# Kernel tuning notes

Measured on AMD Instinct MI355X. Metric: run time of the kernel, lower is better.

Reference implementation:

```python
import jax, jax.numpy as jnp
import numpy as np

B, L, D = 4, 4096, 256


def setup_inputs() -> dict:
    key = jax.random.key(0)
    kx, kq, kk, kv, ko = jax.random.split(key, 5)
    std = 0.02
    return {
        "x": jax.random.normal(kx, (B, L, D), dtype=jnp.float32),
        "Wq": std * jax.random.normal(kq, (D, D), dtype=jnp.float32),
        "Wk": std * jax.random.normal(kk, (D, D), dtype=jnp.float32),
        "Wv": std * jax.random.normal(kv, (D, D), dtype=jnp.float32),
        "Wo": std * jax.random.normal(ko, (D, D), dtype=jnp.float32),
    }


def reference(x, Wq, Wk, Wv, Wo):
    # nn.Linear(d,d,bias=False): y = x @ W.T
    q = x @ Wq.T  # [B,L,D]
    k = x @ Wk.T
    v = x @ Wv.T
    logits = jnp.einsum("bld,bmd->blm", q, k)  # [B,L,L], no 1/sqrt(d) scaling
    Lq = x.shape[1]
    causal_mask = jnp.triu(jnp.ones((Lq, Lq), dtype=bool), k=1)  # True above diag
    # ReLU attention: mask future to 0, relu, divide row i by max(i, 1)
    logits = jnp.where(causal_mask[None], jnp.asarray(0.0, logits.dtype), logits)
    attn = jax.nn.relu(logits)
    row_counts = jnp.maximum(jnp.arange(Lq, dtype=attn.dtype), 1.0)  # clamp_min(1)
    attn = attn / row_counts[None, :, None]
    ctx = jnp.einsum("blm,bmd->bld", attn, v)
    return ctx @ Wo.T
```

## Files before the change

### kernel.cpp

```cpp
#include <hip/hip_runtime.h>

#define BB 4
#define LL 4096
#define DD 256
#define MAXOFF 80

typedef short bf16x8 __attribute__((ext_vector_type(8)));
typedef short bf16x4 __attribute__((ext_vector_type(4)));
typedef float f32x4 __attribute__((ext_vector_type(4)));
typedef unsigned u32x4 __attribute__((ext_vector_type(4)));
typedef unsigned short u16;

__device__ inline u16 f2b(float f) {
    union { float f; unsigned u; } v; v.f = f;
    unsigned r = (v.u + 0x7fffu + ((v.u >> 16) & 1u)) >> 16;
    return (u16)r;
}
__device__ inline float b2f(short s) {
    union { unsigned u; float f; } v; v.u = ((unsigned)(unsigned short)s) << 16;
    return v.f;
}
__device__ inline unsigned pk2(float lo, float hi) {
    union { float f; unsigned u; } a, b; a.f = lo; b.f = hi;
    return __builtin_amdgcn_perm(b.u, a.u, 0x07060302u);
}

__device__ inline f32x4 mfma32(bf16x8 a, bf16x8 b, f32x4 c) {
    return __builtin_amdgcn_mfma_f32_16x16x32_bf16(a, b, c, 0, 0, 0);
}
__device__ inline f32x4 mfma16(bf16x4 a, bf16x4 b, f32x4 c) {
    return __builtin_amdgcn_mfma_f32_16x16x16bf16_1k(a, b, c, 0, 0, 0);
}

__device__ inline void gl_lds(const u16* g, u16* l) {
    __builtin_amdgcn_global_load_lds(
        (const __attribute__((address_space(1))) void*)g,
        (__attribute__((address_space(3))) void*)l, 16, 0, 0);
}


__global__ __launch_bounds__(256) void wconv_kernel(
    const float* __restrict__ Wq, const float* __restrict__ Wk,
    const float* __restrict__ Wv, const float* __restrict__ Wo,
    u16* __restrict__ wf, u16* __restrict__ wo16)
{
    const int w = threadIdx.x >> 6, lane = threadIdx.x & 63;
    const int q4 = lane >> 4, ln = lane & 15;
    const int id = blockIdx.x * 4 + w;
    const int mat = id >> 7, rem = id & 127, ct = rem >> 3, ks = rem & 7;
    if (mat < 3) {
        const float* W = (mat == 0) ? Wq : (mat == 1) ? Wk : Wv;
        const float* src = W + (size_t)(ct * 16 + ln) * DD + ks * 32 + q4 * 8;
        float4 f0 = ((const float4*)src)[0], f1 = ((const float4*)src)[1];
        bf16x8 t;
        t[0] = (short)f2b(f0.x); t[1] = (short)f2b(f0.y);
        t[2] = (short)f2b(f0.z); t[3] = (short)f2b(f0.w);
        t[4] = (short)f2b(f1.x); t[5] = (short)f2b(f1.y);
        t[6] = (short)f2b(f1.z); t[7] = (short)f2b(f1.w);
        *(bf16x8*)(wf + (size_t)mat * 65536 + (ct * 8 + ks) * 512 + lane * 8) = t;
    } else {
        const float* src = Wo + (size_t)(ct * 16 + ln) * DD + ks * 32 + q4 * 4;
        float4 f0 = *(const float4*)src;
        float4 f1 = *(const float4*)(src + 16);
        bf16x4 t0, t1;
        t0[0] = (short)f2b(f0.x); t0[1] = (short)f2b(f0.y);
        t0[2] = (short)f2b(f0.z); t0[3] = (short)f2b(f0.w);
        t1[0] = (short)f2b(f1.x); t1[1] = (short)f2b(f1.y);
        t1[2] = (short)f2b(f1.z); t1[3] = (short)f2b(f1.w);
        *(bf16x4*)(wo16 + (size_t)(ct * 16 + 2 * ks) * 256 + lane * 4) = t0;
        *(bf16x4*)(wo16 + (size_t)(ct * 16 + 2 * ks + 1) * 256 + lane * 4) = t1;
    }
}

__global__ __launch_bounds__(256, 4) void qkv_kernel(
    const float* __restrict__ x, const u16* __restrict__ wf,
    u16* __restrict__ qf, u16* __restrict__ kf_, u16* __restrict__ vf_)
{
    __shared__ u16 lt_q[32 * 136];
    __shared__ u16 lt_k[32 * 136];
    __shared__ u16 lt_v[128 * 40];

    const int w = threadIdx.x >> 6, lane = threadIdx.x & 63;
    const int q4 = lane >> 4, ln = lane & 15;
    const int tg = blockIdx.x >> 1, half = blockIdx.x & 1;
    const int tl = w & 1, dq = w >> 1;

    bf16x8 a[8];
    {
        const float* xrow = x + (size_t)(tg * 32 + tl * 16 + ln) * DD;
        #pragma unroll
        for (int ks = 0; ks < 8; ++ks) {
            const float4* p = (const float4*)(xrow + ks * 32 + q4 * 8);
            float4 f0 = p[0], f1 = p[1];
            bf16x8 t;
            t[0] = (short)f2b(f0.x); t[1] = (short)f2b(f0.y);
            t[2] = (short)f2b(f0.z); t[3] = (short)f2b(f0.w);
            t[4] = (short)f2b(f1.x); t[5] = (short)f2b(f1.y);
            t[6] = (short)f2b(f1.z); t[7] = (short)f2b(f1.w);
            a[ks] = t;
        }
    }

    f32x4 acc0[4], acc1[4], acc2[4];
    #pragma unroll
    for (int cl = 0; cl < 4; ++cl) {
        acc0[cl] = f32x4{0.f, 0.f, 0.f, 0.f};
        acc1[cl] = f32x4{0.f, 0.f, 0.f, 0.f};
        acc2[cl] = f32x4{0.f, 0.f, 0.f, 0.f};
    }

    #pragma unroll
    for (int ks = 0; ks < 8; ++ks) {
        #pragma unroll
        for (int cl = 0; cl < 4; ++cl) {
            const int ct = half * 8 + dq * 4 + cl;
            const size_t off = ((size_t)ct * 8 + ks) * 512 + lane * 8;
            bf16x8 b0 = *(const bf16x8*)(wf + off);
            bf16x8 b1 = *(const bf16x8*)(wf + 65536 + off);
            bf16x8 b2 = *(const bf16x8*)(wf + 131072 + off);
            acc0[cl] = mfma32(a[ks], b0, acc0[cl]);
            acc1[cl] = mfma32(a[ks], b1, acc1[cl]);
            acc2[cl] = mfma32(a[ks], b2, acc2[cl]);
        }
    }

    #pragma unroll
    for (int cl = 0; cl < 4; ++cl) {
        const int coll = (dq * 4 + cl) * 16 + ln;
        #pragma unroll
        for (int r = 0; r < 4; ++r) {
            const int tok = tl * 16 + q4 * 4 + r;
            lt_q[tok * 136 + coll] = f2b(acc0[cl][r]);
            lt_k[tok * 136 + coll] = f2b(acc1[cl][r]);
            lt_v[coll * 40 + tok] = f2b(acc2[cl][r]);
        }
    }
    __syncthreads();

    {
        const int h = w & 1;
        #pragma unroll
        for (int e = 0; e < 2; ++e) {
            const int ksl = 2 * dq + e;
            const int ks = half * 4 + ksl;
            bf16x8 aq = *(const bf16x8*)&lt_q[(h * 16 + ln) * 136 + ksl * 32 + q4 * 8];
            bf16x8 ak = *(const bf16x8*)&lt_k[(h * 16 + ln) * 136 + ksl * 32 + q4 * 8];
            const size_t dst = (size_t)((tg * 2 + h) * 8 + ks) * 512 + lane * 8;
            *(bf16x8*)(qf + dst) = aq;
            *(bf16x8*)(kf_ + dst) = ak;
        }
    }
    #pragma unroll
    for (int e = 0; e < 2; ++e) {
        const int dt_l = 2 * w + e;
        bf16x4 lo = *(const bf16x4*)&lt_v[(dt_l * 16 + ln) * 40 + q4 * 4];
        bf16x4 hi = *(const bf16x4*)&lt_v[(dt_l * 16 + ln) * 40 + 16 + q4 * 4];
        bf16x8 t;
        t[0] = lo[0]; t[1] = lo[1]; t[2] = lo[2]; t[3] = lo[3];
        t[4] = hi[0]; t[5] = hi[1]; t[6] = hi[2]; t[7] = hi[3];
        *(bf16x8*)(vf_ + (size_t)(tg * 16 + half * 8 + dt_l) * 512 + lane * 8) = t;
    }
}

__global__ __launch_bounds__(512, 2) void attn_kernel(
    const u16* __restrict__ qf, const u16* __restrict__ kfr,
    const u16* __restrict__ vfr, u16* __restrict__ part)
{
    __shared__ u16 buf[2][32][512];

    const int id = blockIdx.x;
    const int xcd = id & 7;
    const int b = xcd >> 1;
    const int j = ((xcd & 1) << 5) | (id >> 3);

    const int w = threadIdx.x >> 6, lane = threadIdx.x & 63;
    const int q4 = lane >> 4, ln = lane & 15;

    const int u0 = 17 * j;
    const int u1 = u0 + 17;

    int g = (int)((sqrtf((float)u0 + 1.0f) - 1.0f) * 0.5f);
    while (4 * (g + 1) * (g + 2) <= u0) ++g;
    while (4 * g * (g + 1) > u0) --g;
    int kt = u0 - 4 * g * (g + 1);
    int u = u0;

    int off = 0;
    for (int g2 = 0; g2 < g; ++g2) {
        const int j0 = (4 * g2 * (g2 + 1)) / 17;
        const int jl = (4 * (g2 + 1) * (g2 + 2) - 1) / 17;
        off += jl - j0 + 1;
    }

    {
        const size_t cb = (size_t)((b * 128 + kt) * 16) * 512;
        #pragma unroll
        for (int c4 = 0; c4 < 4; ++c4) {
            const int c = w * 4 + c4;
            const u16* gsrc = ((c < 16) ? (kfr + cb + c * 512)
                                        : (vfr + cb + (c - 16) * 512)) + lane * 8;
            gl_lds(gsrc, &buf[u0 & 1][c][0]);
        }
    }

    while (u < u1) {
        const int ktend = 8 * g + 8;
        const int rem = u1 - u;
        const int kt_stop = (ktend < kt + rem) ? ktend : (kt + rem);
        const int t0 = g * 16 + 2 * w;
        const int qg0 = t0 * 16 + ln;
        const float inv0 = 1.0f / (float)(qg0 > 1 ? qg0 : 1);
        const float inv1 = 1.0f / (float)(qg0 + 16);

        bf16x8 qB0[8], qB1[8];
        {
            const u16* qb0 = qf + (size_t)(t0 * 8) * 512 + (size_t)b * (128 * 16 * 512) + lane * 8;
            #pragma unroll
            for (int ks = 0; ks < 8; ++ks) {
                qB0[ks] = *(const bf16x8*)(qb0 + ks * 512);
                qB1[ks] = *(const bf16x8*)(qb0 + (8 + ks) * 512);
            }
        }

        f32x4 oacc0[16], oacc1[16];
        #pragma unroll
        for (int dt = 0; dt < 16; ++dt) {
            oacc0[dt] = f32x4{0.f, 0.f, 0.f, 0.f};
            oacc1[dt] = f32x4{0.f, 0.f, 0.f, 0.f};
        }

        #pragma unroll 1
        for (; kt < kt_stop; ++kt, ++u) {
            const int cur = u & 1;
            __syncthreads();

            if (u + 1 < u1) {
                const int ktn = (kt + 1 < ktend) ? (kt + 1) : 0;
                const size_t cb = (size_t)((b * 128 + ktn) * 16) * 512;
                #pragma unroll
                for (int c4 = 0; c4 < 4; ++c4) {
                    const int c = w * 4 + c4;
                    const u16* gsrc = ((c < 16) ? (kfr + cb + c * 512)
                                                : (vfr + cb + (c - 16) * 512)) + lane * 8;
                    gl_lds(gsrc, &buf[cur ^ 1][c][0]);
                }
            }

            f32x4 s00 = f32x4{0.f, 0.f, 0.f, 0.f};
            f32x4 s10 = f32x4{0.f, 0.f, 0.f, 0.f};
            f32x4 s01 = f32x4{0.f, 0.f, 0.f, 0.f};
            f32x4 s11 = f32x4{0.f, 0.f, 0.f, 0.f};
            #pragma unroll
            for (int ks = 0; ks < 8; ++ks) {
                bf16x8 kf0 = *(const bf16x8*)&buf[cur][ks][lane * 8];
                bf16x8 kf1 = *(const bf16x8*)&buf[cur][8 + ks][lane * 8];
                s00 = mfma32(kf0, qB0[ks], s00);
                s10 = mfma32(kf1, qB0[ks], s10);
                s01 = mfma32(kf0, qB1[ks], s01);
                s11 = mfma32(kf1, qB1[ks], s11);
            }

            const int d0 = kt * 32 + q4 * 4 - qg0;
            float v00[4], v10[4], v01[4], v11[4];
            #pragma unroll
            for (int rr = 0; rr < 4; ++rr) {
                v00[rr] = (d0 + rr > 0)      ? 0.f : fmaxf(s00[rr], 0.f) * inv0;
                v10[rr] = (d0 + 16 + rr > 0) ? 0.f : fmaxf(s10[rr], 0.f) * inv0;
                v01[rr] = (d0 - 16 + rr > 0) ? 0.f : fmaxf(s01[rr], 0.f) * inv1;
                v11[rr] = (d0 + rr > 0)      ? 0.f : fmaxf(s11[rr], 0.f) * inv1;
            }
            union { u32x4 u; bf16x8 h; } c0, c1;
            c0.u[0] = pk2(v00[0], v00[1]); c0.u[1] = pk2(v00[2], v00[3]);
            c0.u[2] = pk2(v10[0], v10[1]); c0.u[3] = pk2(v10[2], v10[3]);
            c1.u[0] = pk2(v01[0], v01[1]); c1.u[1] = pk2(v01[2], v01[3]);
            c1.u[2] = pk2(v11[0], v11[1]); c1.u[3] = pk2(v11[2], v11[3]);

            #pragma unroll
            for (int dt = 0; dt < 16; ++dt) {
                bf16x8 vv = *(const bf16x8*)&buf[cur][16 + dt][lane * 8];
                oacc0[dt] = mfma32(vv, c0.h, oacc0[dt]);
                oacc1[dt] = mfma32(vv, c1.h, oacc1[dt]);
            }
        }

        {
            const int j0g = (4 * g * (g + 1)) / 17;
            const int gslot = off + (j - j0g);
            u16* pb0 = part + ((((size_t)b * MAXOFF + gslot) * 16 + 2 * w) * 16) * 256 + lane * 4;
            u16* pb1 = pb0 + 16 * 256;
            #pragma unroll
            for (int dt = 0; dt < 16; ++dt) {
                bf16x4 t0v, t1v;
                t0v[0] = (short)f2b(oacc0[dt][0]); t0v[1] = (short)f2b(oacc0[dt][1]);
                t0v[2] = (short)f2b(oacc0[dt][2]); t0v[3] = (short)f2b(oacc0[dt][3]);
                t1v[0] = (short)f2b(oacc1[dt][0]); t1v[1] = (short)f2b(oacc1[dt][1]);
                t1v[2] = (short)f2b(oacc1[dt][2]); t1v[3] = (short)f2b(oacc1[dt][3]);
                *(bf16x4*)(pb0 + dt * 256) = t0v;
                *(bf16x4*)(pb1 + dt * 256) = t1v;
            }
            off += ((4 * (g + 1) * (g + 2) - 1) / 17) - j0g + 1;
        }
        ++g;
        kt = 0;
    }
}

__global__ __launch_bounds__(256, 4) void oproj_kernel(
    const u16* __restrict__ part, const u16* __restrict__ wo16,
    float* __restrict__ out)
{
    __shared__ u16 cb[16 * 256];

    const int w = threadIdx.x >> 6, lane = threadIdx.x & 63;
    const int q4 = lane >> 4, ln = lane & 15;
    const int g16 = blockIdx.x;
    const int b = g16 >> 8, gb = g16 & 255;
    const int g = gb >> 4;
    const int tloc = gb & 15;

    int off = 0;
    for (int g2 = 0; g2 < g; ++g2) {
        const int j0 = (4 * g2 * (g2 + 1)) / 17;
        const int jl = (4 * (g2 + 1) * (g2 + 2) - 1) / 17;
        off += jl - j0 + 1;
    }
    const int j0g = (4 * g * (g + 1)) / 17;
    const int jlg = (4 * (g + 1) * (g + 2) - 1) / 17;
    const int nsl = jlg - j0g + 1;

    #pragma unroll
    for (int c4 = 0; c4 < 4; ++c4) {
        const int dt = w * 4 + c4;
        f32x4 s = f32x4{0.f, 0.f, 0.f, 0.f};
        for (int sl = 0; sl < nsl; ++sl) {
            const u16* p = part + ((((size_t)b * MAXOFF + off + sl) * 16 + tloc) * 16 + dt) * 256 + lane * 4;
            bf16x4 pv = *(const bf16x4*)p;
            s[0] += b2f(pv[0]); s[1] += b2f(pv[1]);
            s[2] += b2f(pv[2]); s[3] += b2f(pv[3]);
        }
        bf16x4 t;
        t[0] = (short)f2b(s[0]); t[1] = (short)f2b(s[1]);
        t[2] = (short)f2b(s[2]); t[3] = (short)f2b(s[3]);
        *(bf16x4*)&cb[dt * 256 + lane * 4] = t;
    }
    __syncthreads();

    #pragma unroll
    for (int c4 = 0; c4 < 4; ++c4) {
        const int ct = w * 4 + c4;
        f32x4 acc = f32x4{0.f, 0.f, 0.f, 0.f};
        #pragma unroll
        for (int dt = 0; dt < 16; ++dt) {
            bf16x4 A = *(const bf16x4*)(wo16 + (size_t)(ct * 16 + dt) * 256 + lane * 4);
            bf16x4 B = *(const bf16x4*)&cb[dt * 256 + lane * 4];
            acc = mfma16(A, B, acc);
        }
        float* o = out + (size_t)(g16 * 16 + ln) * DD + ct * 16 + q4 * 4;
        *(f32x4*)o = acc;
    }
}

extern "C" void kernel_launch(void* const* d_in, const int* in_sizes, int n_in,
                              void* d_out, int out_size, void* d_ws, size_t ws_size,
                              hipStream_t stream)
{
    const float* x  = (const float*)d_in[0];
    const float* Wq = (const float*)d_in[1];
    const float* Wk = (const float*)d_in[2];
    const float* Wv = (const float*)d_in[3];
    const float* Wo = (const float*)d_in[4];
    float* out = (float*)d_out;

    const size_t nW = (size_t)DD * DD;
    const size_t nX = (size_t)BB * LL * DD;

    u16* wf   = (u16*)d_ws;
    u16* wo16 = wf + 3 * nW;
    u16* qfr  = wf + 4 * nW;
    u16* kfr  = qfr + nX;
    u16* vfr  = kfr + nX;
    u16* part = vfr + nX;

    wconv_kernel<<<dim3(128), dim3(256), 0, stream>>>(Wq, Wk, Wv, Wo, wf, wo16);
    qkv_kernel<<<dim3(1024), dim3(256), 0, stream>>>(x, wf, qfr, kfr, vfr);
    attn_kernel<<<dim3(256), dim3(512), 0, stream>>>(qfr, kfr, vfr, part);
    oproj_kernel<<<dim3(1024), dim3(256), 0, stream>>>(part, wo16, out);
}
```

Baseline: 153.9 us.

## Give each attention wave four query tiles, halving the block to four waves

The attention kernel now runs 256 threads (4 waves) per block instead of 512, and each wave handles four 16-row query tiles instead of two. Each K/V fragment read from LDS now feeds twice as many MFMAs, which cuts LDS read traffic per FLOP. Each wave also issues twice as many global-to-LDS copies. The cost is roughly double the accumulator and Q register footprint (64 f32x4 accumulators plus 32 Q fragments per lane) and fewer waves per CU for hiding latency, so register spilling or lower occupancy is a risk.

New measurement: 168.3 us. 9.3% more time.

```diff
diff --git a/kernel.cpp b/kernel.cpp
--- a/kernel.cpp
+++ b/kernel.cpp
@@ -162,7 +162,7 @@
     }
 }
 
-__global__ __launch_bounds__(512, 2) void attn_kernel(
+__global__ __launch_bounds__(256, 1) void attn_kernel(
     const u16* __restrict__ qf, const u16* __restrict__ kfr,
     const u16* __restrict__ vfr, u16* __restrict__ part)
 {
@@ -195,8 +195,8 @@
     {
         const size_t cb = (size_t)((b * 128 + kt) * 16) * 512;
         #pragma unroll
-        for (int c4 = 0; c4 < 4; ++c4) {
-            const int c = w * 4 + c4;
+        for (int c8 = 0; c8 < 8; ++c8) {
+            const int c = w * 8 + c8;
             const u16* gsrc = ((c < 16) ? (kfr + cb + c * 512)
                                         : (vfr + cb + (c - 16) * 512)) + lane * 8;
             gl_lds(gsrc, &buf[u0 & 1][c][0]);
@@ -207,27 +207,31 @@
         const int ktend = 8 * g + 8;
         const int rem = u1 - u;
         const int kt_stop = (ktend < kt + rem) ? ktend : (kt + rem);
-        const int t0 = g * 16 + 2 * w;
+        const int t0 = g * 16 + 4 * w;
         const int qg0 = t0 * 16 + ln;
-        const float inv0 = 1.0f / (float)(qg0 > 1 ? qg0 : 1);
-        const float inv1 = 1.0f / (float)(qg0 + 16);
-
-        bf16x8 qB0[8], qB1[8];
+        float inv[4];
+        inv[0] = 1.0f / (float)(qg0 > 1 ? qg0 : 1);
+        inv[1] = 1.0f / (float)(qg0 + 16);
+        inv[2] = 1.0f / (float)(qg0 + 32);
+        inv[3] = 1.0f / (float)(qg0 + 48);
+
+        bf16x8 qB[4][8];
         {
             const u16* qb0 = qf + (size_t)(t0 * 8) * 512 + (size_t)b * (128 * 16 * 512) + lane * 8;
             #pragma unroll
-            for (int ks = 0; ks < 8; ++ks) {
-                qB0[ks] = *(const bf16x8*)(qb0 + ks * 512);
-                qB1[ks] = *(const bf16x8*)(qb0 + (8 + ks) * 512);
-            }
-        }
-
-        f32x4 oacc0[16], oacc1[16];
-        #pragma unroll
-        for (int dt = 0; dt < 16; ++dt) {
-            oacc0[dt] = f32x4{0.f, 0.f, 0.f, 0.f};
-            oacc1[dt] = f32x4{0.f, 0.f, 0.f, 0.f};
-        }
+            for (int qfg = 0; qfg < 4; ++qfg) {
+                #pragma unroll
+                for (int ks = 0; ks < 8; ++ks)
+                    qB[qfg][ks] = *(const bf16x8*)(qb0 + (qfg * 8 + ks) * 512);
+            }
+        }
+
+        f32x4 oacc[4][16];
+        #pragma unroll
+        for (int qfg = 0; qfg < 4; ++qfg)
+            #pragma unroll
+            for (int dt = 0; dt < 16; ++dt)
+                oacc[qfg][dt] = f32x4{0.f, 0.f, 0.f, 0.f};
 
         #pragma unroll 1
         for (; kt < kt_stop; ++kt, ++u) {
@@ -238,65 +242,69 @@
                 const int ktn = (kt + 1 < ktend) ? (kt + 1) : 0;
                 const size_t cb = (size_t)((b * 128 + ktn) * 16) * 512;
                 #pragma unroll
-                for (int c4 = 0; c4 < 4; ++c4) {
-                    const int c = w * 4 + c4;
+                for (int c8 = 0; c8 < 8; ++c8) {
+                    const int c = w * 8 + c8;
                     const u16* gsrc = ((c < 16) ? (kfr + cb + c * 512)
                                                 : (vfr + cb + (c - 16) * 512)) + lane * 8;
                     gl_lds(gsrc, &buf[cur ^ 1][c][0]);
                 }
             }
 
-            f32x4 s00 = f32x4{0.f, 0.f, 0.f, 0.f};
-            f32x4 s10 = f32x4{0.f, 0.f, 0.f, 0.f};
-            f32x4 s01 = f32x4{0.f, 0.f, 0.f, 0.f};
-            f32x4 s11 = f32x4{0.f, 0.f, 0.f, 0.f};
+            f32x4 s0[4], s1[4];
+            #pragma unroll
+            for (int qfg = 0; qfg < 4; ++qfg) {
+                s0[qfg] = f32x4{0.f, 0.f, 0.f, 0.f};
+                s1[qfg] = f32x4{0.f, 0.f, 0.f, 0.f};
+            }
             #pragma unroll
             for (int ks = 0; ks < 8; ++ks) {
                 bf16x8 kf0 = *(const bf16x8*)&buf[cur][ks][lane * 8];
                 bf16x8 kf1 = *(const bf16x8*)&buf[cur][8 + ks][lane * 8];
-                s00 = mfma32(kf0, qB0[ks], s00);
-                s10 = mfma32(kf1, qB0[ks], s10);
-                s01 = mfma32(kf0, qB1[ks], s01);
-                s11 = mfma32(kf1, qB1[ks], s11);
+                #pragma unroll
+                for (int qfg = 0; qfg < 4; ++qfg) {
+                    s0[qfg] = mfma32(kf0, qB[qfg][ks], s0[qfg]);
+                    s1[qfg] = mfma32(kf1, qB[qfg][ks], s1[qfg]);
+                }
             }
 
             const int d0 = kt * 32 + q4 * 4 - qg0;
-            float v00[4], v10[4], v01[4], v11[4];
-            #pragma unroll
-            for (int rr = 0; rr < 4; ++rr) {
-                v00[rr] = (d0 + rr > 0)      ? 0.f : fmaxf(s00[rr], 0.f) * inv0;
-                v10[rr] = (d0 + 16 + rr > 0) ? 0.f : fmaxf(s10[rr], 0.f) * inv0;
-                v01[rr] = (d0 - 16 + rr > 0) ? 0.f : fmaxf(s01[rr], 0.f) * inv1;
-                v11[rr] = (d0 + rr > 0)      ? 0.f : fmaxf(s11[rr], 0.f) * inv1;
-            }
-            union { u32x4 u; bf16x8 h; } c0, c1;
-            c0.u[0] = pk2(v00[0], v00[1]); c0.u[1] = pk2(v00[2], v00[3]);
-            c0.u[2] = pk2(v10[0], v10[1]); c0.u[3] = pk2(v10[2], v10[3]);
-            c1.u[0] = pk2(v01[0], v01[1]); c1.u[1] = pk2(v01[2], v01[3]);
-            c1.u[2] = pk2(v11[0], v11[1]); c1.u[3] = pk2(v11[2], v11[3]);
+            union { u32x4 u; bf16x8 h; } c[4];
+            #pragma unroll
+            for (int qfg = 0; qfg < 4; ++qfg) {
+                float v0[4], v1[4];
+                #pragma unroll
+                for (int rr = 0; rr < 4; ++rr) {
+                    v0[rr] = (d0 - 16 * qfg + rr > 0)      ? 0.f : fmaxf(s0[qfg][rr], 0.f) * inv[qfg];
+                    v1[rr] = (d0 + 16 - 16 * qfg + rr > 0) ? 0.f : fmaxf(s1[qfg][rr], 0.f) * inv[qfg];
+                }
+                c[qfg].u[0] = pk2(v0[0], v0[1]); c[qfg].u[1] = pk2(v0[2], v0[3]);
+                c[qfg].u[2] = pk2(v1[0], v1[1]); c[qfg].u[3] = pk2(v1[2], v1[3]);
+            }
 
             #pragma unroll
             for (int dt = 0; dt < 16; ++dt) {
                 bf16x8 vv = *(const bf16x8*)&buf[cur][16 + dt][lane * 8];
-                oacc0[dt] = mfma32(vv, c0.h, oacc0[dt]);
-                oacc1[dt] = mfma32(vv, c1.h, oacc1[dt]);
+                #pragma unroll
+                for (int qfg = 0; qfg < 4; ++qfg)
+                    oacc[qfg][dt] = mfma32(vv, c[qfg].h, oacc[qfg][dt]);
             }
         }
 
         {
             const int j0g = (4 * g * (g + 1)) / 17;
             const int gslot = off + (j - j0g);
-            u16* pb0 = part + ((((size_t)b * MAXOFF + gslot) * 16 + 2 * w) * 16) * 256 + lane * 4;
-            u16* pb1 = pb0 + 16 * 256;
-            #pragma unroll
-            for (int dt = 0; dt < 16; ++dt) {
-                bf16x4 t0v, t1v;
-                t0v[0] = (short)f2b(oacc0[dt][0]); t0v[1] = (short)f2b(oacc0[dt][1]);
-                t0v[2] = (short)f2b(oacc0[dt][2]); t0v[3] = (short)f2b(oacc0[dt][3]);
-                t1v[0] = (short)f2b(oacc1[dt][0]); t1v[1] = (short)f2b(oacc1[dt][1]);
-                t1v[2] = (short)f2b(oacc1[dt][2]); t1v[3] = (short)f2b(oacc1[dt][3]);
-                *(bf16x4*)(pb0 + dt * 256) = t0v;
-                *(bf16x4*)(pb1 + dt * 256) = t1v;
+            #pragma unroll
+            for (int qfg = 0; qfg < 4; ++qfg) {
+                u16* pb = part + ((((size_t)b * MAXOFF + gslot) * 16 + (4 * w + qfg)) * 16) * 256 + lane * 4;
+                #pragma unroll
+                for (int dt = 0; dt < 16; ++dt) {
+                    bf16x4 t;
+                    t[0] = (short)f2b(oacc[qfg][dt][0]);
+                    t[1] = (short)f2b(oacc[qfg][dt][1]);
+                    t[2] = (short)f2b(oacc[qfg][dt][2]);
+                    t[3] = (short)f2b(oacc[qfg][dt][3]);
+                    *(bf16x4*)(pb + dt * 256) = t;
+                }
             }
             off += ((4 * (g + 1) * (g + 2) - 1) / 17) - j0g + 1;
         }
@@ -383,6 +391,6 @@
 
     wconv_kernel<<<dim3(128), dim3(256), 0, stream>>>(Wq, Wk, Wv, Wo, wf, wo16);
     qkv_kernel<<<dim3(1024), dim3(256), 0, stream>>>(x, wf, qfr, kfr, vfr);
-    attn_kernel<<<dim3(256), dim3(512), 0, stream>>>(qfr, kfr, vfr, part);
+    attn_kernel<<<dim3(256), dim3(256), 0, stream>>>(qfr, kfr, vfr, part);
     oproj_kernel<<<dim3(1024), dim3(256), 0, stream>>>(part, wo16, out);
 }
```

## Triple-buffer K/V tiles in attention and widen QKV blocks to full width

Applied to the files above, without the earlier changes.

The attention kernel moves from double to triple buffering of K/V tiles. It prefetches two tiles ahead and replaces the per-iteration __syncthreads with an explicit vmcnt wait plus s_barrier, so global loads overlap more with MFMA work. The QKV projection kernel now uses 512-thread blocks that each compute all 256 output columns, so each x row is loaded and converted to bf16 once instead of twice. The trade-off is that the attention kernel now needs 96KB of LDS per block, which may cut blocks per CU. The hand-tuned vmcnt count also depends on how many loads are still in flight.

Measured after the change: 165.1 us. 1.07x slower.

```diff
diff --git a/kernel.cpp b/kernel.cpp
--- a/kernel.cpp
+++ b/kernel.cpp
@@ -72,17 +72,17 @@
     }
 }
 
-__global__ __launch_bounds__(256, 4) void qkv_kernel(
+__global__ __launch_bounds__(512, 2) void qkv_kernel(
     const float* __restrict__ x, const u16* __restrict__ wf,
     u16* __restrict__ qf, u16* __restrict__ kf_, u16* __restrict__ vf_)
 {
-    __shared__ u16 lt_q[32 * 136];
-    __shared__ u16 lt_k[32 * 136];
-    __shared__ u16 lt_v[128 * 40];
+    __shared__ u16 lt_q[32 * 264];
+    __shared__ u16 lt_k[32 * 264];
+    __shared__ u16 lt_v[256 * 40];
 
     const int w = threadIdx.x >> 6, lane = threadIdx.x & 63;
     const int q4 = lane >> 4, ln = lane & 15;
-    const int tg = blockIdx.x >> 1, half = blockIdx.x & 1;
+    const int tg = blockIdx.x;
     const int tl = w & 1, dq = w >> 1;
 
     bf16x8 a[8];
@@ -113,7 +113,7 @@
     for (int ks = 0; ks < 8; ++ks) {
         #pragma unroll
         for (int cl = 0; cl < 4; ++cl) {
-            const int ct = half * 8 + dq * 4 + cl;
+            const int ct = dq * 4 + cl;
             const size_t off = ((size_t)ct * 8 + ks) * 512 + lane * 8;
             bf16x8 b0 = *(const bf16x8*)(wf + off);
             bf16x8 b1 = *(const bf16x8*)(wf + 65536 + off);
@@ -130,21 +130,20 @@
         #pragma unroll
         for (int r = 0; r < 4; ++r) {
             const int tok = tl * 16 + q4 * 4 + r;
-            lt_q[tok * 136 + coll] = f2b(acc0[cl][r]);
-            lt_k[tok * 136 + coll] = f2b(acc1[cl][r]);
+            lt_q[tok * 264 + coll] = f2b(acc0[cl][r]);
+            lt_k[tok * 264 + coll] = f2b(acc1[cl][r]);
             lt_v[coll * 40 + tok] = f2b(acc2[cl][r]);
         }
     }
     __syncthreads();
 
     {
-        const int h = w & 1;
+        const int h = tl;
         #pragma unroll
         for (int e = 0; e < 2; ++e) {
-            const int ksl = 2 * dq + e;
-            const int ks = half * 4 + ksl;
-            bf16x8 aq = *(const bf16x8*)&lt_q[(h * 16 + ln) * 136 + ksl * 32 + q4 * 8];
-            bf16x8 ak = *(const bf16x8*)&lt_k[(h * 16 + ln) * 136 + ksl * 32 + q4 * 8];
+            const int ks = 2 * dq + e;
+            bf16x8 aq = *(const bf16x8*)&lt_q[(h * 16 + ln) * 264 + ks * 32 + q4 * 8];
+            bf16x8 ak = *(const bf16x8*)&lt_k[(h * 16 + ln) * 264 + ks * 32 + q4 * 8];
             const size_t dst = (size_t)((tg * 2 + h) * 8 + ks) * 512 + lane * 8;
             *(bf16x8*)(qf + dst) = aq;
             *(bf16x8*)(kf_ + dst) = ak;
@@ -152,13 +151,13 @@
     }
     #pragma unroll
     for (int e = 0; e < 2; ++e) {
-        const int dt_l = 2 * w + e;
-        bf16x4 lo = *(const bf16x4*)&lt_v[(dt_l * 16 + ln) * 40 + q4 * 4];
-        bf16x4 hi = *(const bf16x4*)&lt_v[(dt_l * 16 + ln) * 40 + 16 + q4 * 4];
+        const int dt = 2 * w + e;
+        bf16x4 lo = *(const bf16x4*)&lt_v[(dt * 16 + ln) * 40 + q4 * 4];
+        bf16x4 hi = *(const bf16x4*)&lt_v[(dt * 16 + ln) * 40 + 16 + q4 * 4];
         bf16x8 t;
         t[0] = lo[0]; t[1] = lo[1]; t[2] = lo[2]; t[3] = lo[3];
         t[4] = hi[0]; t[5] = hi[1]; t[6] = hi[2]; t[7] = hi[3];
-        *(bf16x8*)(vf_ + (size_t)(tg * 16 + half * 8 + dt_l) * 512 + lane * 8) = t;
+        *(bf16x8*)(vf_ + (size_t)(tg * 16 + dt) * 512 + lane * 8) = t;
     }
 }
 
@@ -166,7 +165,7 @@
     const u16* __restrict__ qf, const u16* __restrict__ kfr,
     const u16* __restrict__ vfr, u16* __restrict__ part)
 {
-    __shared__ u16 buf[2][32][512];
+    __shared__ u16 buf[3][32][512];
 
     const int id = blockIdx.x;
     const int xcd = id & 7;
@@ -192,16 +191,23 @@
         off += jl - j0 + 1;
     }
 
-    {
-        const size_t cb = (size_t)((b * 128 + kt) * 16) * 512;
+    int lg = g, lkt = kt;
+    int cur = 0;
+
+    auto issue = [&](int bi) {
+        const size_t cb = (size_t)((b * 128 + lkt) * 16) * 512;
         #pragma unroll
         for (int c4 = 0; c4 < 4; ++c4) {
             const int c = w * 4 + c4;
             const u16* gsrc = ((c < 16) ? (kfr + cb + c * 512)
                                         : (vfr + cb + (c - 16) * 512)) + lane * 8;
-            gl_lds(gsrc, &buf[u0 & 1][c][0]);
-        }
-    }
+            gl_lds(gsrc, &buf[bi][c][0]);
+        }
+        ++lkt; if (lkt == 8 * lg + 8) { lkt = 0; ++lg; }
+    };
+
+    issue(0);
+    if (u0 + 1 < u1) issue(1);
 
     while (u < u1) {
         const int ktend = 8 * g + 8;
@@ -231,19 +237,13 @@
 
         #pragma unroll 1
         for (; kt < kt_stop; ++kt, ++u) {
-            const int cur = u & 1;
-            __syncthreads();
-
-            if (u + 1 < u1) {
-                const int ktn = (kt + 1 < ktend) ? (kt + 1) : 0;
-                const size_t cb = (size_t)((b * 128 + ktn) * 16) * 512;
-                #pragma unroll
-                for (int c4 = 0; c4 < 4; ++c4) {
-                    const int c = w * 4 + c4;
-                    const u16* gsrc = ((c < 16) ? (kfr + cb + c * 512)
-                                                : (vfr + cb + (c - 16) * 512)) + lane * 8;
-                    gl_lds(gsrc, &buf[cur ^ 1][c][0]);
-                }
+            asm volatile("s_waitcnt vmcnt(4)" ::: "memory");
+            __builtin_amdgcn_s_barrier();
+            asm volatile("" ::: "memory");
+
+            if (u + 2 < u1) {
+                const int nb = (cur + 2 >= 3) ? (cur - 1) : (cur + 2);
+                issue(nb);
             }
 
             f32x4 s00 = f32x4{0.f, 0.f, 0.f, 0.f};
@@ -281,6 +281,8 @@
                 oacc0[dt] = mfma32(vv, c0.h, oacc0[dt]);
                 oacc1[dt] = mfma32(vv, c1.h, oacc1[dt]);
             }
+
+            cur = (cur + 1 == 3) ? 0 : (cur + 1);
         }
 
         {
@@ -382,7 +384,7 @@
     u16* part = vfr + nX;
 
     wconv_kernel<<<dim3(128), dim3(256), 0, stream>>>(Wq, Wk, Wv, Wo, wf, wo16);
-    qkv_kernel<<<dim3(1024), dim3(256), 0, stream>>>(x, wf, qfr, kfr, vfr);
+    qkv_kernel<<<dim3(512), dim3(512), 0, stream>>>(x, wf, qfr, kfr, vfr);
     attn_kernel<<<dim3(256), dim3(512), 0, stream>>>(qfr, kfr, vfr, part);
     oproj_kernel<<<dim3(1024), dim3(256), 0, stream>>>(part, wo16, out);
 }
```
